# Performance work log

Measured on AMD Instinct MI355X. Metric: run time of the kernel, lower is better.

The kernel has to match this reference:

```python
import jax, jax.numpy as jnp
import numpy as np

B, C, H, W = 8, 384, 32, 32
NUM_HEADS = 8
HEAD_DIM = C // NUM_HEADS


def setup_inputs() -> dict:
    key = jax.random.key(0)
    k1, k2, k3, k4, k5 = jax.random.split(key, 5)
    s = 1.0 / np.sqrt(C)
    return {
        "x": jax.random.normal(k1, (B, C, H, W), dtype=jnp.float32),
        "w_qkv": jax.random.normal(k2, (3 * C, C), dtype=jnp.float32) * s,   # 1x1 conv == linear over channels
        "b_qkv": jax.random.normal(k3, (3 * C,), dtype=jnp.float32) * 0.01,
        "w_proj": jax.random.normal(k4, (C, C), dtype=jnp.float32) * s,
        "b_proj": jax.random.normal(k5, (C,), dtype=jnp.float32) * 0.01,
    }


def reference(x, w_qkv, b_qkv, w_proj, b_proj):
    b, c, h, w = x.shape
    n = h * w
    scale = HEAD_DIM ** (-0.5)
    # 1x1 conv qkv: (B, 3C, H, W)
    qkv = jnp.einsum('bchw,oc->bohw', x, w_qkv) + b_qkv[None, :, None, None]
    # 'b (three hd d) h0 w0 -> three b hd (h0 w0) d'
    qkv = qkv.reshape(b, 3, NUM_HEADS, HEAD_DIM, n)
    qkv = jnp.transpose(qkv, (1, 0, 2, 4, 3))  # (3, B, heads, N, d)
    q, k, v = qkv[0], qkv[1], qkv[2]
    attn = jnp.einsum('bhnd,bhmd->bhnm', q, k) * scale
    attn = jax.nn.softmax(attn, axis=-1)
    out = jnp.einsum('bhnm,bhmd->bhnd', attn, v)          # (B, heads, N, d)
    out = jnp.transpose(out, (0, 1, 3, 2)).reshape(b, c, h, w)  # b (hd d) h w
    out = jnp.einsum('bchw,oc->bohw', out, w_proj) + b_proj[None, :, None, None]
    return out
```

## Files before the change

kernel.cpp:

```cpp
#include <hip/hip_runtime.h>
#include <hip/hip_bf16.h>

typedef __hip_bfloat16 bf16;
typedef __bf16 bfx8 __attribute__((ext_vector_type(8)));
typedef float f32x4 __attribute__((ext_vector_type(4)));

#define Bk   8
#define Ck   384
#define NHk  8
#define Dk   48
#define Dp   64
#define Nk   1024
#define O3   1152


__global__ __launch_bounds__(256) void xpose_kernel(
    const float* __restrict__ x, bf16* __restrict__ Xs)
{
    __shared__ bf16 tile[32][33];
    const int b = blockIdx.z, c0 = blockIdx.y * 32, n0 = blockIdx.x * 32;
    const int tn = threadIdx.x & 31, tc = threadIdx.x >> 5;
    const float* xb = x + (size_t)b * Ck * Nk;
    #pragma unroll
    for (int i = 0; i < 4; ++i)
        tile[tc + 8 * i][tn] = __float2bfloat16(xb[(size_t)(c0 + tc + 8 * i) * Nk + n0 + tn]);
    __syncthreads();
    bf16* base = Xs + ((size_t)b * 64 + (n0 >> 4)) * 48 * 128 + (c0 >> 3) * 128;
    #pragma unroll
    for (int i = 0; i < 4; ++i) {
        int n_loc = tc + 8 * i, c_loc = tn;
        base[(size_t)(n_loc >> 4) * 6144 + (c_loc >> 3) * 128 +
             (n_loc & 15) * 8 + (c_loc & 7)] = tile[c_loc][n_loc];
    }
}

__global__ __launch_bounds__(256) void wconv_kernel(
    const float* __restrict__ wq, const float* __restrict__ wp,
    bf16* __restrict__ Wq, bf16* __restrict__ Wp,
    bf16* __restrict__ Qs, bf16* __restrict__ Ks)
{
    int i = blockIdx.x * 256 + threadIdx.x;
    if (i < O3 * Ck) {
        int o = i / Ck, c = i - o * Ck;
        Wq[((size_t)(o >> 4) * 48 + (c >> 3)) * 128 + (o & 15) * 8 + (c & 7)] =
            __float2bfloat16(wq[i]);
    }
    if (i < Ck * Ck) {
        int o = i / Ck, c = i - o * Ck;
        Wp[((size_t)(o >> 4) * 48 + (c >> 3)) * 128 + (o & 15) * 8 + (c & 7)] =
            __float2bfloat16(wp[i]);
    }
    if (i < 262144) {
        int buf = i >> 17;
        int r17 = i & 131071;
        int head = r17 >> 11;
        int r11 = r17 & 2047;
        int g = r11 >> 5, c5 = r11 & 31;
        int cd = 6 + (c5 >> 4), e = c5 & 15;
        bf16* p = (buf ? Ks : Qs) + (size_t)head * 65536 +
                  ((size_t)g * 8 + cd) * 128 + e * 8;
        *(int4*)p = (int4){0, 0, 0, 0};
    }
}

__global__ __launch_bounds__(256) void qkv_mfma_kernel(
    const bf16* __restrict__ Xs, const bf16* __restrict__ Wq,
    const float* __restrict__ bias,
    bf16* __restrict__ Qs, bf16* __restrict__ Ks, bf16* __restrict__ Vs)
{
    const int b    = blockIdx.z;
    const int by   = blockIdx.y;
    const int bx   = blockIdx.x;
    const int o0   = by * 64;
    const int n0   = bx * 128;
    const int wave = threadIdx.x >> 6;
    const int lane = threadIdx.x & 63;
    const int l15  = lane & 15, quad = lane >> 4;
    const int t3   = o0 / Ck;

    const bf16* xg[2];
    const bf16* wg[4];
    #pragma unroll
    for (int i = 0; i < 2; ++i)
        xg[i] = Xs + ((size_t)(b * 64 + bx * 8 + wave * 2 + i) * 48) * 128 + lane * 8;
    #pragma unroll
    for (int j = 0; j < 4; ++j)
        wg[j] = Wq + ((size_t)(by * 4 + j) * 48) * 128 + lane * 8;

    f32x4 acc[8];
    #pragma unroll
    for (int i = 0; i < 8; ++i) acc[i] = (f32x4){0.f, 0.f, 0.f, 0.f};

    if (t3 < 2) {
        #pragma unroll
        for (int s = 0; s < 12; ++s) {
            bfx8 fx[2], fw[4];
            #pragma unroll
            for (int i = 0; i < 2; ++i) fx[i] = *(const bfx8*)(xg[i] + s * 512);
            #pragma unroll
            for (int j = 0; j < 4; ++j) fw[j] = *(const bfx8*)(wg[j] + s * 512);
            #pragma unroll
            for (int i = 0; i < 2; ++i)
                #pragma unroll
                for (int j = 0; j < 4; ++j)
                    acc[i * 4 + j] = __builtin_amdgcn_mfma_f32_16x16x32_bf16(
                        fx[i], fw[j], acc[i * 4 + j], 0, 0, 0);
        }
        const float qscale = 0.2082350964f;
        #pragma unroll
        for (int j = 0; j < 4; ++j) {
            int o  = o0 + j * 16 + l15;
            float bi = bias[o];
            int r  = o - t3 * Ck;
            int hd = r / Dk, d = r - hd * Dk;
            bf16* hb = (t3 == 0 ? Qs : Ks) + (size_t)(b * NHk + hd) * 65536
                     + (d >> 3) * 128 + (d & 7);
            #pragma unroll
            for (int i = 0; i < 2; ++i) {
                #pragma unroll
                for (int reg = 0; reg < 4; ++reg) {
                    int npos = n0 + wave * 32 + i * 16 + quad * 4 + reg;
                    float v = acc[i * 4 + j][reg] + bi;
                    if (t3 == 0) v *= qscale;
                    hb[(size_t)(npos >> 4) * 1024 + (npos & 15) * 8] = __float2bfloat16(v);
                }
            }
        }
    } else {
        #pragma unroll
        for (int s = 0; s < 12; ++s) {
            bfx8 fx[2], fw[4];
            #pragma unroll
            for (int i = 0; i < 2; ++i) fx[i] = *(const bfx8*)(xg[i] + s * 512);
            #pragma unroll
            for (int j = 0; j < 4; ++j) fw[j] = *(const bfx8*)(wg[j] + s * 512);
            #pragma unroll
            for (int j = 0; j < 4; ++j)
                #pragma unroll
                for (int i = 0; i < 2; ++i)
                    acc[j * 2 + i] = __builtin_amdgcn_mfma_f32_16x16x32_bf16(
                        fw[j], fx[i], acc[j * 2 + i], 0, 0, 0);
        }
        #pragma unroll
        for (int j = 0; j < 4; ++j) {
            #pragma unroll
            for (int reg = 0; reg < 4; ++reg) {
                int o  = o0 + j * 16 + quad * 4 + reg;
                float bi = bias[o];
                int r  = o - 2 * Ck;
                int hd = r / Dk, d = r - hd * Dk;
                bf16* vb = Vs + (size_t)(b * NHk + hd) * 49152
                         + ((size_t)(d >> 4) * 128) * 128 + (d & 15) * 8;
                #pragma unroll
                for (int i = 0; i < 2; ++i) {
                    int npos = n0 + wave * 32 + i * 16 + l15;
                    vb[(size_t)(npos >> 3) * 128 + (npos & 7)] =
                        __float2bfloat16(acc[j * 2 + i][reg] + bi);
                }
            }
        }
    }
}

__global__ __launch_bounds__(256, 2) void attn_kernel(
    const bf16* __restrict__ Qs, const bf16* __restrict__ Ks,
    const bf16* __restrict__ Vs, bf16* __restrict__ AO)
{
    __shared__ __align__(16) short Ps[4 * 2 * 16 * 72];
    __shared__ float sums[4][2][16];

    const int hd   = blockIdx.x;
    const int b    = blockIdx.y;
    const int bx   = blockIdx.z;
    const int t    = threadIdx.x;
    const int wave = t >> 6;
    const int lane = t & 63;
    const int l15  = lane & 15;
    const int quad = lane >> 4;
    const int grp16 = (bx * 4 + wave) * 2;

    const bf16* qb = Qs + (size_t)(b * NHk + hd) * 65536;
    const bf16* kb = Ks + (size_t)(b * NHk + hd) * 65536;
    const bf16* vb = Vs + (size_t)(b * NHk + hd) * 49152;

    bfx8 bq[2][2];
    #pragma unroll
    for (int qt = 0; qt < 2; ++qt) {
        const bf16* qp = qb + ((size_t)(grp16 + qt) * 8 + quad) * 128 + l15 * 8;
        bq[qt][0] = *(const bfx8*)(qp);
        bq[qt][1] = *(const bfx8*)(qp + 512);
    }

    float l_run[2] = {0.f, 0.f};
    f32x4 oacc[2][3];
    #pragma unroll
    for (int qt = 0; qt < 2; ++qt)
        #pragma unroll
        for (int dc = 0; dc < 3; ++dc) oacc[qt][dc] = (f32x4){0.f, 0.f, 0.f, 0.f};

    short* const PsW[2] = { Ps + wave * 2304, Ps + wave * 2304 + 1152 };

    auto loadK = [&](bfx8* kf, int k0) {
        const bf16* kp0 = kb + (size_t)k0 * 64 + quad * 128 + l15 * 8;
        #pragma unroll
        for (int s = 0; s < 4; ++s) {
            kf[2 * s]     = *(const bfx8*)(kp0 + s * 1024);
            kf[2 * s + 1] = *(const bfx8*)(kp0 + s * 1024 + 512);
        }
    };
    auto loadV = [&](bfx8* vf, int k0) {
        const bf16* vp0 = vb + ((size_t)(k0 >> 3) + quad) * 128 + l15 * 8;
        #pragma unroll
        for (int dc = 0; dc < 3; ++dc) {
            vf[2 * dc]     = *(const bfx8*)(vp0 + (size_t)dc * 16384);
            vf[2 * dc + 1] = *(const bfx8*)(vp0 + (size_t)dc * 16384 + 512);
        }
    };

    auto step = [&](const bfx8* kf, bfx8* kfn, int k0, bool pf) {
        bfx8 vf[6];
        loadV(vf, k0);
        if (pf) loadK(kfn, k0 + 64);

        f32x4 sf[2][4];
        #pragma unroll
        for (int s = 0; s < 4; ++s) {
            #pragma unroll
            for (int qt = 0; qt < 2; ++qt) {
                f32x4 z = (f32x4){0.f, 0.f, 0.f, 0.f};
                z = __builtin_amdgcn_mfma_f32_16x16x32_bf16(kf[2 * s],     bq[qt][0], z, 0, 0, 0);
                z = __builtin_amdgcn_mfma_f32_16x16x32_bf16(kf[2 * s + 1], bq[qt][1], z, 0, 0, 0);
                sf[qt][s] = z;
            }
        }

        #pragma unroll
        for (int qt = 0; qt < 2; ++qt) {
            float lsum = 0.f;
            #pragma unroll
            for (int s = 0; s < 4; ++s) {
                ushort4 pk;
                float e0 = __builtin_amdgcn_exp2f(sf[qt][s][0]);
                float e1 = __builtin_amdgcn_exp2f(sf[qt][s][1]);
                float e2 = __builtin_amdgcn_exp2f(sf[qt][s][2]);
                float e3 = __builtin_amdgcn_exp2f(sf[qt][s][3]);
                lsum += (e0 + e1) + (e2 + e3);
                bf16 h0 = __float2bfloat16(e0), h1 = __float2bfloat16(e1);
                bf16 h2 = __float2bfloat16(e2), h3 = __float2bfloat16(e3);
                pk.x = *(unsigned short*)&h0; pk.y = *(unsigned short*)&h1;
                pk.z = *(unsigned short*)&h2; pk.w = *(unsigned short*)&h3;
                *(ushort4*)&PsW[qt][l15 * 72 + s * 16 + quad * 4] = pk;
            }
            l_run[qt] += lsum;
        }

        #pragma unroll
        for (int qt = 0; qt < 2; ++qt) {
            const bfx8 ap0 = *(const bfx8*)&PsW[qt][l15 * 72 + quad * 8];
            const bfx8 ap1 = *(const bfx8*)&PsW[qt][l15 * 72 + 32 + quad * 8];
            #pragma unroll
            for (int dc = 0; dc < 3; ++dc) {
                oacc[qt][dc] = __builtin_amdgcn_mfma_f32_16x16x32_bf16(
                    ap0, vf[2 * dc], oacc[qt][dc], 0, 0, 0);
                oacc[qt][dc] = __builtin_amdgcn_mfma_f32_16x16x32_bf16(
                    ap1, vf[2 * dc + 1], oacc[qt][dc], 0, 0, 0);
            }
        }
    };

    bfx8 kfA[8], kfB[8];
    loadK(kfA, 0);
    #pragma unroll 1
    for (int k0 = 0; k0 < Nk; k0 += 128) {
        step(kfA, kfB, k0, true);
        step(kfB, kfA, k0 + 64, k0 + 128 < Nk);
    }

    #pragma unroll
    for (int qt = 0; qt < 2; ++qt) {
        float lt = l_run[qt];
        lt += __shfl_xor(lt, 16, 64);
        lt += __shfl_xor(lt, 32, 64);
        sums[wave][qt][l15] = lt;
    }

    #pragma unroll
    for (int qt = 0; qt < 2; ++qt) {
        short* OsW = PsW[qt];
        #pragma unroll
        for (int r = 0; r < 4; ++r) {
            int qi = quad * 4 + r;
            float rli = 1.0f / sums[wave][qt][qi];
            #pragma unroll
            for (int dcc = 0; dcc < 3; ++dcc) {
                bf16 hb = __float2bfloat16(oacc[qt][dcc][r] * rli);
                OsW[qi * 64 + dcc * 16 + l15] = *(short*)&hb;
            }
        }
    }

    #pragma unroll
    for (int qt = 0; qt < 2; ++qt) {
        bf16* aob = AO + (((size_t)b * 64 + grp16 + qt) * 48 + hd * 6) * 128;
        short* OsW = PsW[qt];
        int u = lane;
        int4 v = *(const int4*)&OsW[(u & 15) * 64 + (u >> 4) * 8];
        *(int4*)(aob + u * 8) = v;
        if (lane < 32) {
            int u2 = 64 + lane;
            int4 v2 = *(const int4*)&OsW[(u2 & 15) * 64 + (u2 >> 4) * 8];
            *(int4*)(aob + u2 * 8) = v2;
        }
    }
}

__global__ __launch_bounds__(256) void proj_mfma_kernel(
    const bf16* __restrict__ AO, const bf16* __restrict__ Wp,
    const float* __restrict__ bias, float* __restrict__ out)
{
    const int b    = blockIdx.z;
    const int by   = blockIdx.y;
    const int bx   = blockIdx.x;
    const int o0   = by * 64;
    const int n0   = bx * 128;
    const int wave = threadIdx.x >> 6;
    const int lane = threadIdx.x & 63;
    const int l15  = lane & 15, quad = lane >> 4;

    const bf16* ag[2];
    const bf16* wg[4];
    #pragma unroll
    for (int i = 0; i < 2; ++i)
        ag[i] = AO + ((size_t)(b * 64 + bx * 8 + wave * 2 + i) * 48) * 128 + lane * 8;
    #pragma unroll
    for (int j = 0; j < 4; ++j)
        wg[j] = Wp + ((size_t)(by * 4 + j) * 48) * 128 + lane * 8;

    f32x4 acc[8];
    #pragma unroll
    for (int i = 0; i < 8; ++i) acc[i] = (f32x4){0.f, 0.f, 0.f, 0.f};

    #pragma unroll
    for (int s = 0; s < 12; ++s) {
        bfx8 fx[2], fw[4];
        #pragma unroll
        for (int i = 0; i < 2; ++i) fx[i] = *(const bfx8*)(ag[i] + s * 512);
        #pragma unroll
        for (int j = 0; j < 4; ++j) fw[j] = *(const bfx8*)(wg[j] + s * 512);
        #pragma unroll
        for (int j = 0; j < 4; ++j)
            #pragma unroll
            for (int i = 0; i < 2; ++i)
                acc[j * 2 + i] = __builtin_amdgcn_mfma_f32_16x16x32_bf16(
                    fw[j], fx[i], acc[j * 2 + i], 0, 0, 0);
    }

    #pragma unroll
    for (int j = 0; j < 4; ++j) {
        #pragma unroll
        for (int reg = 0; reg < 4; ++reg) {
            int o  = o0 + j * 16 + quad * 4 + reg;
            float bi = bias[o];
            #pragma unroll
            for (int i = 0; i < 2; ++i) {
                int npos = n0 + wave * 32 + i * 16 + l15;
                out[((size_t)b * Ck + o) * Nk + npos] = acc[j * 2 + i][reg] + bi;
            }
        }
    }
}

extern "C" void kernel_launch(void* const* d_in, const int* in_sizes, int n_in,
                              void* d_out, int out_size, void* d_ws, size_t ws_size,
                              hipStream_t stream)
{
    const float* x      = (const float*)d_in[0];
    const float* w_qkv  = (const float*)d_in[1];
    const float* b_qkv  = (const float*)d_in[2];
    const float* w_proj = (const float*)d_in[3];
    const float* b_proj = (const float*)d_in[4];
    float* out = (float*)d_out;

    const size_t XT_SEG = (size_t)Bk * Nk * Ck;
    const size_t WQ_SEG = (size_t)O3 * Ck;
    const size_t WP_SEG = (size_t)Ck * Ck;
    const size_t QK_SEG = (size_t)Bk * NHk * Nk * Dp;
    const size_t V_SEG  = (size_t)Bk * NHk * Dk * Nk;

    bf16* Xs = (bf16*)d_ws;
    bf16* Wq = Xs + XT_SEG;
    bf16* Wp = Wq + WQ_SEG;
    bf16* Qs = Wp + WP_SEG;
    bf16* Ks = Qs + QK_SEG;
    bf16* Vs = Ks + QK_SEG;
    bf16* AO = Vs + V_SEG;

    xpose_kernel<<<dim3(Nk / 32, Ck / 32, Bk), 256, 0, stream>>>(x, Xs);
    wconv_kernel<<<(O3 * Ck + 255) / 256, 256, 0, stream>>>(
        w_qkv, w_proj, Wq, Wp, Qs, Ks);
    qkv_mfma_kernel<<<dim3(Nk / 128, O3 / 64, Bk), 256, 0, stream>>>(
        Xs, Wq, b_qkv, Qs, Ks, Vs);
    attn_kernel<<<dim3(NHk, Bk, 8), 256, 0, stream>>>(Qs, Ks, Vs, AO);
    proj_mfma_kernel<<<dim3(Nk / 128, Ck / 64, Bk), 256, 0, stream>>>(
        AO, Wp, b_proj, out);
}
```

Baseline: 125.8 us.

## Stage K/V and weight tiles in LDS via direct global-to-LDS loads; merge prep kernels

Merges the transpose and weight-conversion kernels into a single launch. The QKV and projection GEMMs now load their 64-row weight slab into shared memory with global_load_lds before the MFMA loop, so the four waves no longer each fetch the same weights from global memory. The attention kernel double-buffers K and V tiles in LDS, prefetching the next tile while computing the current one, and replaces the per-wave register prefetch. This adds block-wide barriers, a full vmcnt wait every step, and more LDS per block, which may reduce occupancy.

```diff
diff --git a/kernel.cpp b/kernel.cpp
--- a/kernel.cpp
+++ b/kernel.cpp
@@ -14,52 +14,60 @@
 #define O3   1152
 
 
-__global__ __launch_bounds__(256) void xpose_kernel(
-    const float* __restrict__ x, bf16* __restrict__ Xs)
-{
-    __shared__ bf16 tile[32][33];
-    const int b = blockIdx.z, c0 = blockIdx.y * 32, n0 = blockIdx.x * 32;
-    const int tn = threadIdx.x & 31, tc = threadIdx.x >> 5;
-    const float* xb = x + (size_t)b * Ck * Nk;
-    #pragma unroll
-    for (int i = 0; i < 4; ++i)
-        tile[tc + 8 * i][tn] = __float2bfloat16(xb[(size_t)(c0 + tc + 8 * i) * Nk + n0 + tn]);
-    __syncthreads();
-    bf16* base = Xs + ((size_t)b * 64 + (n0 >> 4)) * 48 * 128 + (c0 >> 3) * 128;
-    #pragma unroll
-    for (int i = 0; i < 4; ++i) {
-        int n_loc = tc + 8 * i, c_loc = tn;
-        base[(size_t)(n_loc >> 4) * 6144 + (c_loc >> 3) * 128 +
-             (n_loc & 15) * 8 + (c_loc & 7)] = tile[c_loc][n_loc];
-    }
-}
-
-__global__ __launch_bounds__(256) void wconv_kernel(
+__device__ __forceinline__ void gload_lds16(const bf16* src, void* dst)
+{
+    __builtin_amdgcn_global_load_lds(
+        (const __attribute__((address_space(1))) void*)src,
+        (__attribute__((address_space(3))) void*)dst, 16, 0, 0);
+}
+
+__global__ __launch_bounds__(256) void prep_kernel(
+    const float* __restrict__ x, bf16* __restrict__ Xs,
     const float* __restrict__ wq, const float* __restrict__ wp,
     bf16* __restrict__ Wq, bf16* __restrict__ Wp,
     bf16* __restrict__ Qs, bf16* __restrict__ Ks)
 {
-    int i = blockIdx.x * 256 + threadIdx.x;
-    if (i < O3 * Ck) {
-        int o = i / Ck, c = i - o * Ck;
-        Wq[((size_t)(o >> 4) * 48 + (c >> 3)) * 128 + (o & 15) * 8 + (c & 7)] =
-            __float2bfloat16(wq[i]);
-    }
-    if (i < Ck * Ck) {
-        int o = i / Ck, c = i - o * Ck;
-        Wp[((size_t)(o >> 4) * 48 + (c >> 3)) * 128 + (o & 15) * 8 + (c & 7)] =
-            __float2bfloat16(wp[i]);
-    }
-    if (i < 262144) {
-        int buf = i >> 17;
-        int r17 = i & 131071;
-        int head = r17 >> 11;
-        int r11 = r17 & 2047;
-        int g = r11 >> 5, c5 = r11 & 31;
-        int cd = 6 + (c5 >> 4), e = c5 & 15;
-        bf16* p = (buf ? Ks : Qs) + (size_t)head * 65536 +
-                  ((size_t)g * 8 + cd) * 128 + e * 8;
-        *(int4*)p = (int4){0, 0, 0, 0};
+    __shared__ bf16 tile[32][33];
+    if (blockIdx.x < 3072) {
+        const int id = blockIdx.x;
+        const int b = id / 384, rem = id % 384;
+        const int c0 = ((rem >> 5) % 12) * 32, n0 = (rem & 31) * 32;
+        const int tn = threadIdx.x & 31, tc = threadIdx.x >> 5;
+        const float* xb = x + (size_t)b * Ck * Nk;
+        #pragma unroll
+        for (int i = 0; i < 4; ++i)
+            tile[tc + 8 * i][tn] = __float2bfloat16(xb[(size_t)(c0 + tc + 8 * i) * Nk + n0 + tn]);
+        __syncthreads();
+        bf16* base = Xs + ((size_t)b * 64 + (n0 >> 4)) * 48 * 128 + (c0 >> 3) * 128;
+        #pragma unroll
+        for (int i = 0; i < 4; ++i) {
+            int n_loc = tc + 8 * i, c_loc = tn;
+            base[(size_t)(n_loc >> 4) * 6144 + (c_loc >> 3) * 128 +
+                 (n_loc & 15) * 8 + (c_loc & 7)] = tile[c_loc][n_loc];
+        }
+    } else {
+        int i = (blockIdx.x - 3072) * 256 + threadIdx.x;
+        if (i < O3 * Ck) {
+            int o = i / Ck, c = i - o * Ck;
+            Wq[((size_t)(o >> 4) * 48 + (c >> 3)) * 128 + (o & 15) * 8 + (c & 7)] =
+                __float2bfloat16(wq[i]);
+        }
+        if (i < Ck * Ck) {
+            int o = i / Ck, c = i - o * Ck;
+            Wp[((size_t)(o >> 4) * 48 + (c >> 3)) * 128 + (o & 15) * 8 + (c & 7)] =
+                __float2bfloat16(wp[i]);
+        }
+        if (i < 262144) {
+            int buf = i >> 17;
+            int r17 = i & 131071;
+            int head = r17 >> 11;
+            int r11 = r17 & 2047;
+            int g = r11 >> 5, c5 = r11 & 31;
+            int cd = 6 + (c5 >> 4), e = c5 & 15;
+            bf16* p = (buf ? Ks : Qs) + (size_t)head * 65536 +
+                      ((size_t)g * 8 + cd) * 128 + e * 8;
+            *(int4*)p = (int4){0, 0, 0, 0};
+        }
     }
 }
 
@@ -68,6 +76,8 @@
     const float* __restrict__ bias,
     bf16* __restrict__ Qs, bf16* __restrict__ Ks, bf16* __restrict__ Vs)
 {
+    __shared__ __align__(16) bf16 Wl[24576];
+
     const int b    = blockIdx.z;
     const int by   = blockIdx.y;
     const int bx   = blockIdx.x;
@@ -78,18 +88,27 @@
     const int l15  = lane & 15, quad = lane >> 4;
     const int t3   = o0 / Ck;
 
+    {
+        const bf16* wsrc = Wq + (size_t)by * 24576;
+        #pragma unroll
+        for (int i = 0; i < 12; ++i) {
+            int f = wave * 12 + i;
+            gload_lds16(wsrc + f * 512 + lane * 8, (char*)Wl + f * 1024);
+        }
+    }
+
     const bf16* xg[2];
-    const bf16* wg[4];
     #pragma unroll
     for (int i = 0; i < 2; ++i)
         xg[i] = Xs + ((size_t)(b * 64 + bx * 8 + wave * 2 + i) * 48) * 128 + lane * 8;
-    #pragma unroll
-    for (int j = 0; j < 4; ++j)
-        wg[j] = Wq + ((size_t)(by * 4 + j) * 48) * 128 + lane * 8;
+    const bf16* wl = Wl + lane * 8;
 
     f32x4 acc[8];
     #pragma unroll
     for (int i = 0; i < 8; ++i) acc[i] = (f32x4){0.f, 0.f, 0.f, 0.f};
+
+    asm volatile("s_waitcnt vmcnt(0)" ::: "memory");
+    __syncthreads();
 
     if (t3 < 2) {
         #pragma unroll
@@ -98,7 +117,7 @@
             #pragma unroll
             for (int i = 0; i < 2; ++i) fx[i] = *(const bfx8*)(xg[i] + s * 512);
             #pragma unroll
-            for (int j = 0; j < 4; ++j) fw[j] = *(const bfx8*)(wg[j] + s * 512);
+            for (int j = 0; j < 4; ++j) fw[j] = *(const bfx8*)(wl + j * 6144 + s * 512);
             #pragma unroll
             for (int i = 0; i < 2; ++i)
                 #pragma unroll
@@ -133,7 +152,7 @@
             #pragma unroll
             for (int i = 0; i < 2; ++i) fx[i] = *(const bfx8*)(xg[i] + s * 512);
             #pragma unroll
-            for (int j = 0; j < 4; ++j) fw[j] = *(const bfx8*)(wg[j] + s * 512);
+            for (int j = 0; j < 4; ++j) fw[j] = *(const bfx8*)(wl + j * 6144 + s * 512);
             #pragma unroll
             for (int j = 0; j < 4; ++j)
                 #pragma unroll
@@ -166,7 +185,9 @@
     const bf16* __restrict__ Qs, const bf16* __restrict__ Ks,
     const bf16* __restrict__ Vs, bf16* __restrict__ AO)
 {
-    __shared__ __align__(16) short Ps[4 * 2 * 16 * 72];
+    __shared__ __align__(16) bf16 KbL[2][4096];
+    __shared__ __align__(16) bf16 VbL[2][3072];
+    __shared__ __align__(16) short Ps[4 * 2 * 1152];
     __shared__ float sums[4][2][16];
 
     const int hd   = blockIdx.x;
@@ -183,6 +204,32 @@
     const bf16* kb = Ks + (size_t)(b * NHk + hd) * 65536;
     const bf16* vb = Vs + (size_t)(b * NHk + hd) * 49152;
 
+    auto stage = [&](int buf, int k0) {
+        const bf16* ksrc = kb + (size_t)k0 * 64;
+        const bf16* vsrc = vb + (size_t)(k0 >> 3) * 128;
+        char* kdst = (char*)&KbL[buf][0];
+        char* vdst = (char*)&VbL[buf][0];
+        #pragma unroll
+        for (int i = 0; i < 4; ++i) {
+            const int l = wave + i * 4;
+            if (l < 14) {
+                const int piece = l >> 1, half = l & 1;
+                const bf16* src; char* dst;
+                if (piece < 4) {
+                    src = ksrc + piece * 1024 + half * 512 + lane * 8;
+                    dst = kdst + piece * 2048 + half * 1024;
+                } else {
+                    const int dc = piece - 4;
+                    src = vsrc + (size_t)dc * 16384 + half * 512 + lane * 8;
+                    dst = vdst + dc * 2048 + half * 1024;
+                }
+                gload_lds16(src, dst);
+            }
+        }
+    };
+
+    stage(0, 0);
+
     bfx8 bq[2][2];
     #pragma unroll
     for (int qt = 0; qt < 2; ++qt) {
@@ -199,37 +246,27 @@
         for (int dc = 0; dc < 3; ++dc) oacc[qt][dc] = (f32x4){0.f, 0.f, 0.f, 0.f};
 
     short* const PsW[2] = { Ps + wave * 2304, Ps + wave * 2304 + 1152 };
-
-    auto loadK = [&](bfx8* kf, int k0) {
-        const bf16* kp0 = kb + (size_t)k0 * 64 + quad * 128 + l15 * 8;
+    const int lo = quad * 128 + l15 * 8;
+
+    asm volatile("s_waitcnt vmcnt(0)" ::: "memory");
+    __syncthreads();
+
+    auto step = [&](int buf, int k0, bool pf) {
+        if (pf) stage(buf ^ 1, k0 + 64);
+
+        const bf16* Kc = &KbL[buf][0];
+        const bf16* Vc = &VbL[buf][0];
+
+        f32x4 sf[2][4];
         #pragma unroll
         for (int s = 0; s < 4; ++s) {
-            kf[2 * s]     = *(const bfx8*)(kp0 + s * 1024);
-            kf[2 * s + 1] = *(const bfx8*)(kp0 + s * 1024 + 512);
-        }
-    };
-    auto loadV = [&](bfx8* vf, int k0) {
-        const bf16* vp0 = vb + ((size_t)(k0 >> 3) + quad) * 128 + l15 * 8;
-        #pragma unroll
-        for (int dc = 0; dc < 3; ++dc) {
-            vf[2 * dc]     = *(const bfx8*)(vp0 + (size_t)dc * 16384);
-            vf[2 * dc + 1] = *(const bfx8*)(vp0 + (size_t)dc * 16384 + 512);
-        }
-    };
-
-    auto step = [&](const bfx8* kf, bfx8* kfn, int k0, bool pf) {
-        bfx8 vf[6];
-        loadV(vf, k0);
-        if (pf) loadK(kfn, k0 + 64);
-
-        f32x4 sf[2][4];
-        #pragma unroll
-        for (int s = 0; s < 4; ++s) {
+            const bfx8 kf0 = *(const bfx8*)(Kc + s * 1024 + lo);
+            const bfx8 kf1 = *(const bfx8*)(Kc + s * 1024 + 512 + lo);
             #pragma unroll
             for (int qt = 0; qt < 2; ++qt) {
                 f32x4 z = (f32x4){0.f, 0.f, 0.f, 0.f};
-                z = __builtin_amdgcn_mfma_f32_16x16x32_bf16(kf[2 * s],     bq[qt][0], z, 0, 0, 0);
-                z = __builtin_amdgcn_mfma_f32_16x16x32_bf16(kf[2 * s + 1], bq[qt][1], z, 0, 0, 0);
+                z = __builtin_amdgcn_mfma_f32_16x16x32_bf16(kf0, bq[qt][0], z, 0, 0, 0);
+                z = __builtin_amdgcn_mfma_f32_16x16x32_bf16(kf1, bq[qt][1], z, 0, 0, 0);
                 sf[qt][s] = z;
             }
         }
@@ -260,20 +297,23 @@
             const bfx8 ap1 = *(const bfx8*)&PsW[qt][l15 * 72 + 32 + quad * 8];
             #pragma unroll
             for (int dc = 0; dc < 3; ++dc) {
+                const bfx8 bv0 = *(const bfx8*)(Vc + dc * 1024 + lo);
+                const bfx8 bv1 = *(const bfx8*)(Vc + dc * 1024 + 512 + lo);
                 oacc[qt][dc] = __builtin_amdgcn_mfma_f32_16x16x32_bf16(
-                    ap0, vf[2 * dc], oacc[qt][dc], 0, 0, 0);
+                    ap0, bv0, oacc[qt][dc], 0, 0, 0);
                 oacc[qt][dc] = __builtin_amdgcn_mfma_f32_16x16x32_bf16(
-                    ap1, vf[2 * dc + 1], oacc[qt][dc], 0, 0, 0);
-            }
-        }
+                    ap1, bv1, oacc[qt][dc], 0, 0, 0);
+            }
+        }
+
+        asm volatile("s_waitcnt vmcnt(0)" ::: "memory");
+        __syncthreads();
     };
 
-    bfx8 kfA[8], kfB[8];
-    loadK(kfA, 0);
     #pragma unroll 1
     for (int k0 = 0; k0 < Nk; k0 += 128) {
-        step(kfA, kfB, k0, true);
-        step(kfB, kfA, k0 + 64, k0 + 128 < Nk);
+        step(0, k0, true);
+        step(1, k0 + 64, k0 + 128 < Nk);
     }
 
     #pragma unroll
@@ -318,6 +358,8 @@
     const bf16* __restrict__ AO, const bf16* __restrict__ Wp,
     const float* __restrict__ bias, float* __restrict__ out)
 {
+    __shared__ __align__(16) bf16 Wl[24576];
+
     const int b    = blockIdx.z;
     const int by   = blockIdx.y;
     const int bx   = blockIdx.x;
@@ -327,18 +369,27 @@
     const int lane = threadIdx.x & 63;
     const int l15  = lane & 15, quad = lane >> 4;
 
+    {
+        const bf16* wsrc = Wp + (size_t)by * 24576;
+        #pragma unroll
+        for (int i = 0; i < 12; ++i) {
+            int f = wave * 12 + i;
+            gload_lds16(wsrc + f * 512 + lane * 8, (char*)Wl + f * 1024);
+        }
+    }
+
     const bf16* ag[2];
-    const bf16* wg[4];
     #pragma unroll
     for (int i = 0; i < 2; ++i)
         ag[i] = AO + ((size_t)(b * 64 + bx * 8 + wave * 2 + i) * 48) * 128 + lane * 8;
-    #pragma unroll
-    for (int j = 0; j < 4; ++j)
-        wg[j] = Wp + ((size_t)(by * 4 + j) * 48) * 128 + lane * 8;
+    const bf16* wl = Wl + lane * 8;
 
     f32x4 acc[8];
     #pragma unroll
     for (int i = 0; i < 8; ++i) acc[i] = (f32x4){0.f, 0.f, 0.f, 0.f};
+
+    asm volatile("s_waitcnt vmcnt(0)" ::: "memory");
+    __syncthreads();
 
     #pragma unroll
     for (int s = 0; s < 12; ++s) {
@@ -346,7 +397,7 @@
         #pragma unroll
         for (int i = 0; i < 2; ++i) fx[i] = *(const bfx8*)(ag[i] + s * 512);
         #pragma unroll
-        for (int j = 0; j < 4; ++j) fw[j] = *(const bfx8*)(wg[j] + s * 512);
+        for (int j = 0; j < 4; ++j) fw[j] = *(const bfx8*)(wl + j * 6144 + s * 512);
         #pragma unroll
         for (int j = 0; j < 4; ++j)
             #pragma unroll
@@ -395,9 +446,8 @@
     bf16* Vs = Ks + QK_SEG;
     bf16* AO = Vs + V_SEG;
 
-    xpose_kernel<<<dim3(Nk / 32, Ck / 32, Bk), 256, 0, stream>>>(x, Xs);
-    wconv_kernel<<<(O3 * Ck + 255) / 256, 256, 0, stream>>>(
-        w_qkv, w_proj, Wq, Wp, Qs, Ks);
+    prep_kernel<<<3072 + (O3 * Ck + 255) / 256, 256, 0, stream>>>(
+        x, Xs, w_qkv, w_proj, Wq, Wp, Qs, Ks);
     qkv_mfma_kernel<<<dim3(Nk / 128, O3 / 64, Bk), 256, 0, stream>>>(
         Xs, Wq, b_qkv, Qs, Ks, Vs);
     attn_kernel<<<dim3(NHk, Bk, 8), 256, 0, stream>>>(Qs, Ks, Vs, AO);
```

After: 120.5 us. 4.2% less time.
